# Performance work log

Hardware: AMD Instinct MI355X
Metric: run time of the kernel (lower is better)

Reference implementation:

```python
import jax, jax.numpy as jnp
import numpy as np

B, S, D = 2, 2048, 1024
H, KS = 16, 64

def setup_inputs() -> dict:
    key = jax.random.key(0)
    k1, k2, k3, k4, k5 = jax.random.split(key, 5)
    return {
        "x": jax.random.normal(k1, (B, S, D), dtype=jnp.float32),
        "Wq": jax.random.normal(k2, (D, KS, H), dtype=jnp.float32) * 0.02,
        "Wk": jax.random.normal(k3, (D, KS, H), dtype=jnp.float32) * 0.02,
        "Wv": jax.random.normal(k4, (D, KS, H), dtype=jnp.float32) * 0.02,
        "kernel": jax.random.normal(k5, (H * KS, KS), dtype=jnp.float32) * 0.02,
    }

def reference(x, Wq, Wk, Wv, kernel):
    b, s, d = x.shape
    ks, h = Wq.shape[1], Wq.shape[2]
    # projections: heads-last layout [b, s, ks, h]
    q = jnp.einsum('bsd,dkh->bskh', x, Wq)
    k = jnp.einsum('bsd,dkh->bskh', x, Wk)
    v = jnp.einsum('bsd,dkh->bskh', x, Wv)
    # scores [b, i(query), l(key), h]
    scores = jnp.einsum('bikh,blkh->bilh', q, k) / jnp.sqrt(jnp.float32(ks))
    # strictly-upper-triangular (future) mask, as in the original:
    # band_part(ones,0,-1) - eye  ->  1 where l > i
    li = jnp.arange(s)
    mask = (li[None, :] > li[:, None]).astype(jnp.float32)  # [s, s]
    scores = scores - 1e8 * mask[None, :, :, None]
    weights = jax.nn.softmax(scores, axis=2)  # softmax over key axis l
    heads = jnp.einsum('bilh,blkh->bikh', weights, v)  # [b, s, ks, h]
    heads = heads.reshape(b, s, ks * h)  # row-major flatten of (ks, h), matching tf.reshape
    return heads @ kernel  # [b, s, ks]
```

## Files before the change

### kernel.cpp

```cpp
#include <hip/hip_runtime.h>
#include <hip/hip_bf16.h>

#define BB 2
#define SS 2048
#define DD 1024
#define HH 16
#define KSZ 64

typedef __attribute__((ext_vector_type(8))) short s16x8;
typedef __attribute__((ext_vector_type(4))) float f32x4;
typedef __attribute__((ext_vector_type(8))) unsigned short u16x8;
typedef __attribute__((ext_vector_type(4))) unsigned short u16x4;
typedef __attribute__((ext_vector_type(2))) unsigned int u32x2;
typedef unsigned short u16;

__device__ __forceinline__ u16 bf16rne(float f) {
  unsigned int u = __float_as_uint(f);
  unsigned int r = (u + 0x7FFFu + ((u >> 16) & 1u)) >> 16;
  return (u16)r;
}

__device__ __forceinline__ void lds_dma16(const u16* g, u16* l) {
  __builtin_amdgcn_global_load_lds(
      (const __attribute__((address_space(1))) unsigned int*)(const void*)g,
      (__attribute__((address_space(3))) unsigned int*)(void*)l, 16, 0, 0);
}

__global__ __launch_bounds__(256) void prep_all(
    const float* __restrict__ x, const float* __restrict__ Wq,
    const float* __restrict__ Wk, const float* __restrict__ Wv,
    const float* __restrict__ kern, u16* __restrict__ xb,
    u16* __restrict__ Wt, u16* __restrict__ BpT) {
  __shared__ float Ts[64][65];
  const int bid = blockIdx.x;
  const int tid = threadIdx.x;
  if (bid < 2048) {
    int idx = (bid * 256 + tid) * 8;
    float4 a = *(const float4*)(x + idx);
    float4 b = *(const float4*)(x + idx + 4);
    u16x8 v;
    v[0] = bf16rne(a.x); v[1] = bf16rne(a.y); v[2] = bf16rne(a.z); v[3] = bf16rne(a.w);
    v[4] = bf16rne(b.x); v[5] = bf16rne(b.y); v[6] = bf16rne(b.z); v[7] = bf16rne(b.w);
    *(u16x8*)(xb + idx) = v;
  } else if (bid < 2816) {
    const int bx = bid - 2048;
    const int p = bx >> 8, rem = bx & 255;
    const int d0 = (rem & 15) * 64, n0 = (rem >> 4) * 64;
    const float* W = (p == 0) ? Wq : (p == 1) ? Wk : Wv;
    u16* Wo = Wt + (size_t)p * DD * DD;
    #pragma unroll
    for (int i = 0; i < 4; ++i) {
      int f4 = tid + i * 256;
      int r = f4 >> 4, c4 = f4 & 15;
      float4 v = *(const float4*)(W + (size_t)(d0 + r) * DD + n0 + c4 * 4);
      Ts[r][c4 * 4 + 0] = v.x; Ts[r][c4 * 4 + 1] = v.y;
      Ts[r][c4 * 4 + 2] = v.z; Ts[r][c4 * 4 + 3] = v.w;
    }
    __syncthreads();
    #pragma unroll
    for (int i = 0; i < 4; ++i) {
      int ch = tid + i * 256;
      int n = ch >> 4, d4 = ch & 15;
      u16x4 o;
      #pragma unroll
      for (int j = 0; j < 4; ++j) o[j] = bf16rne(Ts[d4 * 4 + j][n]);
      *(u16x4*)(Wo + (size_t)(n0 + n) * DD + d0 + d4 * 4) = o;
    }
  } else {
    const int n = bid - 2816;
    const int k4 = tid * 4;
    u16x4 o;
    #pragma unroll
    for (int j = 0; j < 4; ++j) {
      int kp = k4 + j;
      int h = kp >> 6, k = kp & 63;
      o[j] = bf16rne(kern[(size_t)(k * HH + h) * KSZ + n]);
    }
    *(u16x4*)(BpT + (size_t)n * (HH * KSZ) + k4) = o;
  }
}

__global__ __launch_bounds__(256) void proj_kernel(
    const u16* __restrict__ xb, const u16* __restrict__ Wt,
    u16* __restrict__ qkvT) {
  const int xcd = blockIdx.x & 7;
  const int idx = blockIdx.x >> 3;
  const int mt = (xcd >> 1) * 8 + (idx & 7);
  const int nt = (xcd & 1) * 4 + ((idx >> 3) & 3);
  const int p  = idx >> 5;
  const int m0 = mt * 128, n0 = nt * 128;
  const u16* W = Wt + (size_t)p * DD * DD;
  u16* outp = qkvT + (size_t)p * (BB * HH * SS * KSZ);

  __shared__ __align__(16) unsigned char raw[34816];
  u16* As0 = (u16*)raw;
  u16* Bs0 = As0 + 128 * 32;
  u16* As1 = Bs0 + 128 * 32;
  u16* Bs1 = As1 + 128 * 32;
  u16* Cs  = (u16*)raw;

  const int tid = threadIdx.x;
  const int wave = tid >> 6, lane = tid & 63;
  const int g = lane >> 4, c = lane & 15;
  const int mbase = (wave & 1) * 64, nbase = (wave >> 1) * 64;

  const int lr = lane >> 2, lc = lane & 3;
  const int swz = (lc ^ ((lr >> 1) & 3)) * 8;
  const int rA0 = (wave * 2 + 0) * 16;
  const int rA1 = (wave * 2 + 1) * 16;
  const u16* srcA0 = xb + (size_t)(m0 + rA0 + lr) * DD + swz;
  const u16* srcA1 = xb + (size_t)(m0 + rA1 + lr) * DD + swz;
  const u16* srcB0 = W  + (size_t)(n0 + rA0 + lr) * DD + swz;
  const u16* srcB1 = W  + (size_t)(n0 + rA1 + lr) * DD + swz;
  const int sl0 = rA0 * 32, sl1 = rA1 * 32;

  f32x4 acc[4][4];
  #pragma unroll
  for (int i = 0; i < 4; ++i)
    #pragma unroll
    for (int j = 0; j < 4; ++j) acc[i][j] = {0.f, 0.f, 0.f, 0.f};

  lds_dma16(srcA0, As0 + sl0);  lds_dma16(srcA1, As0 + sl1);
  lds_dma16(srcB0, Bs0 + sl0);  lds_dma16(srcB1, Bs0 + sl1);
  __syncthreads();

  const int jsw = (c >> 1) & 3;
  #pragma unroll 2
  for (int t = 0; t < 32; ++t) {
    u16* Ac = (t & 1) ? As1 : As0;
    u16* Bc = (t & 1) ? Bs1 : Bs0;
    if (t < 31) {
      u16* An = (t & 1) ? As0 : As1;
      u16* Bn = (t & 1) ? Bs0 : Bs1;
      const int ko = (t + 1) * 32;
      lds_dma16(srcA0 + ko, An + sl0);  lds_dma16(srcA1 + ko, An + sl1);
      lds_dma16(srcB0 + ko, Bn + sl0);  lds_dma16(srcB1 + ko, Bn + sl1);
    }
    s16x8 af[4], bfr[4];
    #pragma unroll
    for (int mf = 0; mf < 4; ++mf)
      af[mf] = *(const s16x8*)&Ac[(mbase + mf * 16 + c) * 32 + ((g ^ jsw) * 8)];
    #pragma unroll
    for (int nf = 0; nf < 4; ++nf)
      bfr[nf] = *(const s16x8*)&Bc[(nbase + nf * 16 + c) * 32 + ((g ^ jsw) * 8)];
    #pragma unroll
    for (int mf = 0; mf < 4; ++mf)
      #pragma unroll
      for (int nf = 0; nf < 4; ++nf)
        acc[mf][nf] = __builtin_amdgcn_mfma_f32_16x16x32_bf16(
            af[mf], bfr[nf], acc[mf][nf], 0, 0, 0);
    __syncthreads();
  }

  const float cscale = (p == 0) ? 0.125f * 1.44269504f : 1.0f;
  #pragma unroll
  for (int mf = 0; mf < 4; ++mf)
    #pragma unroll
    for (int nf = 0; nf < 4; ++nf)
      #pragma unroll
      for (int r = 0; r < 4; ++r)
        Cs[(mbase + mf * 16 + g * 4 + r) * 136 + nbase + nf * 16 + c] =
            bf16rne(acc[mf][nf][r] * cscale);
  __syncthreads();
  const int b = m0 >> 11;
  if (p < 2) {
    int hh = tid >> 4, si = tid & 15;
    #pragma unroll
    for (int i = 0; i < 8; ++i) {
      int row = i * 16 + si;
      int s = (m0 + row) & 2047;
      u16x8 v;
      #pragma unroll
      for (int kp = 0; kp < 8; ++kp) v[kp] = Cs[row * 136 + kp * 16 + hh];
      *(u16x8*)(outp + ((size_t)(b * HH + hh) * SS + s) * KSZ + (n0 >> 4)) = v;
    }
  } else {
    const int s0 = m0 & 2047;
    #pragma unroll
    for (int i = 0; i < 8; ++i) {
      int chunk = tid + i * 256;
      int colid = chunk >> 4;
      int hh = colid >> 3, kp = colid & 7;
      int s8 = chunk & 15;
      u16x8 v;
      #pragma unroll
      for (int j = 0; j < 8; ++j) v[j] = Cs[(s8 * 8 + j) * 136 + kp * 16 + hh];
      *(u16x8*)(outp + ((size_t)(b * HH + hh) * KSZ + (n0 >> 4) + kp) * SS +
                s0 + s8 * 8) = v;
    }
  }
}

__global__ __launch_bounds__(256) void attn_kernel(
    const u16* __restrict__ qkvT, u16* __restrict__ headsB) {
  const int bid = blockIdx.x;
  const int hb = bid & 31;
  const int u  = bid >> 5;
  const int it = (u & 1) ? (31 - (u >> 1)) : (u >> 1);
  const int h = hb & 15, b = hb >> 4;
  const size_t plane = (size_t)(b * HH + h) * SS * KSZ;
  const size_t PSZ = (size_t)BB * HH * SS * KSZ;
  const u16* Qg = qkvT + plane;
  const u16* Kg = qkvT + PSZ + plane;
  const u16* Vg = qkvT + 2 * PSZ + plane;

  __shared__ u16 Ks[2][64 * 64];
  __shared__ u16 Vt[2][64 * 64];
  __shared__ u16 Ps[64 * 64];

  const int tid = threadIdx.x;
  const int wave = tid >> 6, lane = tid & 63;
  const int g = lane >> 4, c = lane & 15;
  const int wq0 = wave * 16;

  const int lr = lane >> 3, sc = lane & 7;
  const int r0 = wave * 8;
  const int swz = (sc ^ lr) * 8;
  const u16* Ksrc0 = Kg + (size_t)(r0 + lr) * KSZ + swz;
  const u16* Ksrc1 = Kg + (size_t)(r0 + 32 + lr) * KSZ + swz;
  const u16* Vsrc0 = Vg + (size_t)(r0 + lr) * SS + swz;
  const u16* Vsrc1 = Vg + (size_t)(r0 + 32 + lr) * SS + swz;
  const int d0 = r0 * 64, d1 = (r0 + 32) * 64;

  s16x8 bq0 = *(const s16x8*)(Qg + (size_t)(it * 64 + wq0 + c) * KSZ + g * 8);
  s16x8 bq1 = *(const s16x8*)(Qg + (size_t)(it * 64 + wq0 + c) * KSZ + 32 + g * 8);

  lds_dma16(Ksrc0, &Ks[0][d0]);  lds_dma16(Ksrc1, &Ks[0][d1]);
  lds_dma16(Vsrc0, &Vt[0][d0]);  lds_dma16(Vsrc1, &Vt[0][d1]);
  __syncthreads();

  f32x4 o[4];
  #pragma unroll
  for (int mf = 0; mf < 4; ++mf) o[mf] = {0.f, 0.f, 0.f, 0.f};
  float l_i = 0.f;
  const int cswz = c & 7;

  #pragma unroll 1
  for (int t = 0; t <= it; ++t) {
    const int buf = t & 1;
    if (t < it) {
      const int nb = buf ^ 1;
      const int ko = (t + 1) * 64;
      lds_dma16(Ksrc0 + (size_t)ko * KSZ, &Ks[nb][d0]);
      lds_dma16(Ksrc1 + (size_t)ko * KSZ, &Ks[nb][d1]);
      lds_dma16(Vsrc0 + ko, &Vt[nb][d0]);
      lds_dma16(Vsrc1 + ko, &Vt[nb][d1]);
    }
    f32x4 s[4];
    #pragma unroll
    for (int mf = 0; mf < 4; ++mf) s[mf] = {0.f, 0.f, 0.f, 0.f};
    #pragma unroll
    for (int ks = 0; ks < 2; ++ks) {
      const s16x8 bq = ks ? bq1 : bq0;
      #pragma unroll
      for (int mf = 0; mf < 4; ++mf) {
        s16x8 ak = *(const s16x8*)&Ks[buf][(mf * 16 + c) * 64 +
                                          (((ks * 4 + g) ^ cswz) * 8)];
        s[mf] = __builtin_amdgcn_mfma_f32_16x16x32_bf16(ak, bq, s[mf], 0, 0, 0);
      }
    }
    if (t == it) {
      const int qloc = wq0 + c;
      #pragma unroll
      for (int mf = 0; mf < 4; ++mf)
        #pragma unroll
        for (int r = 0; r < 4; ++r)
          if (mf * 16 + g * 4 + r > qloc) s[mf][r] = -1e30f;
    }
    float ps = 0.f;
    #pragma unroll
    for (int mf = 0; mf < 4; ++mf) {
      float p0 = __builtin_amdgcn_exp2f(s[mf][0]);
      float p1 = __builtin_amdgcn_exp2f(s[mf][1]);
      float p2 = __builtin_amdgcn_exp2f(s[mf][2]);
      float p3 = __builtin_amdgcn_exp2f(s[mf][3]);
      ps += (p0 + p1) + (p2 + p3);
      u32x2 d;
      d[0] = (__float_as_uint(p0) >> 16) | (__float_as_uint(p1) & 0xFFFF0000u);
      d[1] = (__float_as_uint(p2) >> 16) | (__float_as_uint(p3) & 0xFFFF0000u);
      *(u32x2*)&Ps[(wq0 + c) * 64 + (((mf * 2 + (g >> 1)) ^ cswz) * 8) +
                   ((g & 1) * 4)] = d;
    }
    l_i += ps;
    #pragma unroll
    for (int ks = 0; ks < 2; ++ks) {
      s16x8 bp = *(const s16x8*)&Ps[(wq0 + c) * 64 + (((ks * 4 + g) ^ cswz) * 8)];
      #pragma unroll
      for (int mf = 0; mf < 4; ++mf) {
        s16x8 av = *(const s16x8*)&Vt[buf][(mf * 16 + c) * 64 +
                                           (((ks * 4 + g) ^ cswz) * 8)];
        o[mf] = __builtin_amdgcn_mfma_f32_16x16x32_bf16(av, bp, o[mf], 0, 0, 0);
      }
    }
    __syncthreads();
  }
  l_i += __shfl_xor(l_i, 16);
  l_i += __shfl_xor(l_i, 32);
  const float inv = 1.0f / l_i;
  const int q = it * 64 + wq0 + c;
  #pragma unroll
  for (int mf = 0; mf < 4; ++mf) {
    u16x4 hv;
    #pragma unroll
    for (int r = 0; r < 4; ++r) hv[r] = bf16rne(o[mf][r] * inv);
    *(u16x4*)(headsB + plane + (size_t)q * KSZ + mf * 16 + g * 4) = hv;
  }
}

__global__ __launch_bounds__(256) void out_kernel(
    const u16* __restrict__ headsB, const u16* __restrict__ BpT,
    float* __restrict__ out) {
  const int m0 = blockIdx.x * 16;
  const int tid = threadIdx.x;
  const int wave = tid >> 6, lane = tid & 63;
  const int g = lane >> 4, c = lane & 15;

  const int m = m0 + c;
  const int b = m >> 11, s = m & 2047;

  f32x4 acc[4];
  #pragma unroll
  for (int nf = 0; nf < 4; ++nf) acc[nf] = {0.f, 0.f, 0.f, 0.f};

  #pragma unroll
  for (int it = 0; it < 8; ++it) {
    const int kb = wave * 256 + it * 32;
    const int hh = kb >> 6, kk = (kb & 63) + g * 8;
    s16x8 a = *(const s16x8*)(headsB +
        ((size_t)(b * HH + hh) * SS + s) * KSZ + kk);
    #pragma unroll
    for (int nf = 0; nf < 4; ++nf) {
      s16x8 bf = *(const s16x8*)(BpT +
          (size_t)(nf * 16 + c) * (HH * KSZ) + kb + g * 8);
      acc[nf] = __builtin_amdgcn_mfma_f32_16x16x32_bf16(a, bf, acc[nf], 0, 0, 0);
    }
  }

  __shared__ __align__(16) float red[4][64][16];
  #pragma unroll
  for (int nf = 0; nf < 4; ++nf)
    *(f32x4*)&red[wave][lane][nf * 4] = acc[nf];
  __syncthreads();

  const int mi = tid >> 4, n4 = (tid & 15) * 4;
  const int gg = mi >> 2, rr = mi & 3;
  float4 res;
  float* rp = &res.x;
  #pragma unroll
  for (int j = 0; j < 4; ++j) {
    int n = n4 + j;
    int cc = n & 15, nf = n >> 4;
    rp[j] = red[0][gg * 16 + cc][nf * 4 + rr] + red[1][gg * 16 + cc][nf * 4 + rr] +
            red[2][gg * 16 + cc][nf * 4 + rr] + red[3][gg * 16 + cc][nf * 4 + rr];
  }
  *(float4*)(out + (size_t)(m0 + mi) * KSZ + n4) = res;
}

extern "C" void kernel_launch(void* const* d_in, const int* in_sizes, int n_in,
                              void* d_out, int out_size, void* d_ws, size_t ws_size,
                              hipStream_t stream) {
  const float* x    = (const float*)d_in[0];
  const float* Wq   = (const float*)d_in[1];
  const float* Wk   = (const float*)d_in[2];
  const float* Wv   = (const float*)d_in[3];
  const float* kern = (const float*)d_in[4];
  float* out = (float*)d_out;

  u16* xb     = (u16*)d_ws;
  u16* Wt     = xb + (size_t)4096 * 1024;
  u16* qkvT   = Wt + (size_t)3 * 1024 * 1024;
  u16* headsB = qkvT + (size_t)3 * BB * HH * SS * KSZ;
  u16* BpT    = headsB + (size_t)BB * HH * SS * KSZ;

  prep_all<<<dim3(2880), 256, 0, stream>>>(x, Wq, Wk, Wv, kern, xb, Wt, BpT);
  proj_kernel<<<dim3(768), 256, 0, stream>>>(xb, Wt, qkvT);
  attn_kernel<<<dim3(1024), 256, 0, stream>>>(qkvT, headsB);
  out_kernel<<<dim3(256), 256, 0, stream>>>(headsB, BpT, out);
}
```

Measured before the change: 166.0 us.

## Process two adjacent query tiles per 512-thread block sharing K/V loads

The attention kernel now launches 512-thread blocks, each handling two consecutive 64-row query tiles (itB-1 and itB) with 8 waves. The two tiles share the double-buffered K/V tiles in LDS, which roughly halves K/V global traffic. The LDS DMA loads are replaced by register-staged prefetch, loading one tile ahead into registers and storing it to LDS the next iteration. The waves on the lower tile go idle for the last iteration, and the grid is half as large, which may reduce load balance and occupancy.

```diff
diff --git a/kernel.cpp b/kernel.cpp
--- a/kernel.cpp
+++ b/kernel.cpp
@@ -191,12 +191,13 @@
   }
 }
 
-__global__ __launch_bounds__(256) void attn_kernel(
+__global__ __launch_bounds__(512) void attn_kernel(
     const u16* __restrict__ qkvT, u16* __restrict__ headsB) {
   const int bid = blockIdx.x;
   const int hb = bid & 31;
-  const int u  = bid >> 5;
-  const int it = (u & 1) ? (31 - (u >> 1)) : (u >> 1);
+  const int uu = bid >> 5;
+  const int p  = (uu < 8) ? uu : 23 - uu;
+  const int itB = 2 * p + 1;
   const int h = hb & 15, b = hb >> 4;
   const size_t plane = (size_t)(b * HH + h) * SS * KSZ;
   const size_t PSZ = (size_t)BB * HH * SS * KSZ;
@@ -206,27 +207,28 @@
 
   __shared__ u16 Ks[2][64 * 64];
   __shared__ u16 Vt[2][64 * 64];
-  __shared__ u16 Ps[64 * 64];
+  __shared__ u16 Ps[128 * 64];
 
   const int tid = threadIdx.x;
   const int wave = tid >> 6, lane = tid & 63;
   const int g = lane >> 4, c = lane & 15;
-  const int wq0 = wave * 16;
-
-  const int lr = lane >> 3, sc = lane & 7;
-  const int r0 = wave * 8;
-  const int swz = (sc ^ lr) * 8;
-  const u16* Ksrc0 = Kg + (size_t)(r0 + lr) * KSZ + swz;
-  const u16* Ksrc1 = Kg + (size_t)(r0 + 32 + lr) * KSZ + swz;
-  const u16* Vsrc0 = Vg + (size_t)(r0 + lr) * SS + swz;
-  const u16* Vsrc1 = Vg + (size_t)(r0 + 32 + lr) * SS + swz;
-  const int d0 = r0 * 64, d1 = (r0 + 32) * 64;
-
-  s16x8 bq0 = *(const s16x8*)(Qg + (size_t)(it * 64 + wq0 + c) * KSZ + g * 8);
-  s16x8 bq1 = *(const s16x8*)(Qg + (size_t)(it * 64 + wq0 + c) * KSZ + 32 + g * 8);
-
-  lds_dma16(Ksrc0, &Ks[0][d0]);  lds_dma16(Ksrc1, &Ks[0][d1]);
-  lds_dma16(Vsrc0, &Vt[0][d0]);  lds_dma16(Vsrc1, &Vt[0][d1]);
+  const int wq0 = (wave & 3) * 16;
+  const int myIt = itB - ((wave < 4) ? 1 : 0);
+  const int pq0 = wave * 16;
+  const int sr = tid >> 3, sc = tid & 7;
+  const int so = sr * 64 + ((sc ^ (sr & 7)) * 8);
+
+  s16x8 bq0 = *(const s16x8*)(Qg + (size_t)(myIt * 64 + wq0 + c) * KSZ + g * 8);
+  s16x8 bq1 = *(const s16x8*)(Qg + (size_t)(myIt * 64 + wq0 + c) * KSZ + 32 + g * 8);
+
+  u16x8 kr = *(const u16x8*)(Kg + (size_t)sr * KSZ + sc * 8);
+  u16x8 vr = *(const u16x8*)(Vg + (size_t)sr * SS + sc * 8);
+  *(u16x8*)&Ks[0][so] = kr;
+  *(u16x8*)&Vt[0][so] = vr;
+  if (itB >= 1) {
+    kr = *(const u16x8*)(Kg + (size_t)(64 + sr) * KSZ + sc * 8);
+    vr = *(const u16x8*)(Vg + (size_t)sr * SS + 64 + sc * 8);
+  }
   __syncthreads();
 
   f32x4 o[4];
@@ -236,60 +238,65 @@
   const int cswz = c & 7;
 
   #pragma unroll 1
-  for (int t = 0; t <= it; ++t) {
+  for (int t = 0; t <= itB; ++t) {
     const int buf = t & 1;
-    if (t < it) {
+    if (t < itB) {
       const int nb = buf ^ 1;
-      const int ko = (t + 1) * 64;
-      lds_dma16(Ksrc0 + (size_t)ko * KSZ, &Ks[nb][d0]);
-      lds_dma16(Ksrc1 + (size_t)ko * KSZ, &Ks[nb][d1]);
-      lds_dma16(Vsrc0 + ko, &Vt[nb][d0]);
-      lds_dma16(Vsrc1 + ko, &Vt[nb][d1]);
-    }
-    f32x4 s[4];
-    #pragma unroll
-    for (int mf = 0; mf < 4; ++mf) s[mf] = {0.f, 0.f, 0.f, 0.f};
-    #pragma unroll
-    for (int ks = 0; ks < 2; ++ks) {
-      const s16x8 bq = ks ? bq1 : bq0;
+      *(u16x8*)&Ks[nb][so] = kr;
+      *(u16x8*)&Vt[nb][so] = vr;
+      if (t + 2 <= itB) {
+        const int kv2 = t + 2;
+        kr = *(const u16x8*)(Kg + (size_t)(kv2 * 64 + sr) * KSZ + sc * 8);
+        vr = *(const u16x8*)(Vg + (size_t)sr * SS + kv2 * 64 + sc * 8);
+      }
+    }
+    if (t <= myIt) {
+      f32x4 s[4];
+      #pragma unroll
+      for (int mf = 0; mf < 4; ++mf) s[mf] = {0.f, 0.f, 0.f, 0.f};
+      #pragma unroll
+      for (int ks = 0; ks < 2; ++ks) {
+        const s16x8 bq = ks ? bq1 : bq0;
+        #pragma unroll
+        for (int mf = 0; mf < 4; ++mf) {
+          s16x8 ak = *(const s16x8*)&Ks[buf][(mf * 16 + c) * 64 +
+                                            (((ks * 4 + g) ^ cswz) * 8)];
+          s[mf] = __builtin_amdgcn_mfma_f32_16x16x32_bf16(ak, bq, s[mf], 0, 0, 0);
+        }
+      }
+      if (t == myIt) {
+        const int qloc = wq0 + c;
+        #pragma unroll
+        for (int mf = 0; mf < 4; ++mf)
+          #pragma unroll
+          for (int r = 0; r < 4; ++r)
+            if (mf * 16 + g * 4 + r > qloc) s[mf][r] = -1e30f;
+      }
+      float ps = 0.f;
       #pragma unroll
       for (int mf = 0; mf < 4; ++mf) {
-        s16x8 ak = *(const s16x8*)&Ks[buf][(mf * 16 + c) * 64 +
-                                          (((ks * 4 + g) ^ cswz) * 8)];
-        s[mf] = __builtin_amdgcn_mfma_f32_16x16x32_bf16(ak, bq, s[mf], 0, 0, 0);
-      }
-    }
-    if (t == it) {
-      const int qloc = wq0 + c;
-      #pragma unroll
-      for (int mf = 0; mf < 4; ++mf)
+        float p0 = __builtin_amdgcn_exp2f(s[mf][0]);
+        float p1 = __builtin_amdgcn_exp2f(s[mf][1]);
+        float p2 = __builtin_amdgcn_exp2f(s[mf][2]);
+        float p3 = __builtin_amdgcn_exp2f(s[mf][3]);
+        ps += (p0 + p1) + (p2 + p3);
+        u32x2 d;
+        d[0] = (__float_as_uint(p0) >> 16) | (__float_as_uint(p1) & 0xFFFF0000u);
+        d[1] = (__float_as_uint(p2) >> 16) | (__float_as_uint(p3) & 0xFFFF0000u);
+        *(u32x2*)&Ps[(pq0 + c) * 64 + (((mf * 2 + (g >> 1)) ^ cswz) * 8) +
+                     ((g & 1) * 4)] = d;
+      }
+      l_i += ps;
+      #pragma unroll
+      for (int ks = 0; ks < 2; ++ks) {
+        s16x8 bp = *(const s16x8*)&Ps[(pq0 + c) * 64 +
+                                      (((ks * 4 + g) ^ cswz) * 8)];
         #pragma unroll
-        for (int r = 0; r < 4; ++r)
-          if (mf * 16 + g * 4 + r > qloc) s[mf][r] = -1e30f;
-    }
-    float ps = 0.f;
-    #pragma unroll
-    for (int mf = 0; mf < 4; ++mf) {
-      float p0 = __builtin_amdgcn_exp2f(s[mf][0]);
-      float p1 = __builtin_amdgcn_exp2f(s[mf][1]);
-      float p2 = __builtin_amdgcn_exp2f(s[mf][2]);
-      float p3 = __builtin_amdgcn_exp2f(s[mf][3]);
-      ps += (p0 + p1) + (p2 + p3);
-      u32x2 d;
-      d[0] = (__float_as_uint(p0) >> 16) | (__float_as_uint(p1) & 0xFFFF0000u);
-      d[1] = (__float_as_uint(p2) >> 16) | (__float_as_uint(p3) & 0xFFFF0000u);
-      *(u32x2*)&Ps[(wq0 + c) * 64 + (((mf * 2 + (g >> 1)) ^ cswz) * 8) +
-                   ((g & 1) * 4)] = d;
-    }
-    l_i += ps;
-    #pragma unroll
-    for (int ks = 0; ks < 2; ++ks) {
-      s16x8 bp = *(const s16x8*)&Ps[(wq0 + c) * 64 + (((ks * 4 + g) ^ cswz) * 8)];
-      #pragma unroll
-      for (int mf = 0; mf < 4; ++mf) {
-        s16x8 av = *(const s16x8*)&Vt[buf][(mf * 16 + c) * 64 +
-                                           (((ks * 4 + g) ^ cswz) * 8)];
-        o[mf] = __builtin_amdgcn_mfma_f32_16x16x32_bf16(av, bp, o[mf], 0, 0, 0);
+        for (int mf = 0; mf < 4; ++mf) {
+          s16x8 av = *(const s16x8*)&Vt[buf][(mf * 16 + c) * 64 +
+                                             (((ks * 4 + g) ^ cswz) * 8)];
+          o[mf] = __builtin_amdgcn_mfma_f32_16x16x32_bf16(av, bp, o[mf], 0, 0, 0);
+        }
       }
     }
     __syncthreads();
@@ -297,7 +304,7 @@
   l_i += __shfl_xor(l_i, 16);
   l_i += __shfl_xor(l_i, 32);
   const float inv = 1.0f / l_i;
-  const int q = it * 64 + wq0 + c;
+  const int q = myIt * 64 + wq0 + c;
   #pragma unroll
   for (int mf = 0; mf < 4; ++mf) {
     u16x4 hv;
@@ -374,6 +381,6 @@
 
   prep_all<<<dim3(2880), 256, 0, stream>>>(x, Wq, Wk, Wv, kern, xb, Wt, BpT);
   proj_kernel<<<dim3(768), 256, 0, stream>>>(xb, Wt, qkvT);
-  attn_kernel<<<dim3(1024), 256, 0, stream>>>(qkvT, headsB);
+  attn_kernel<<<dim3(512), 512, 0, stream>>>(qkvT, headsB);
   out_kernel<<<dim3(256), 256, 0, stream>>>(headsB, BpT, out);
 }
```

Measured after the change: 162.1 us. 1.02x faster.
